# Kernel tuning notes

Hardware: AMD Instinct MI355X
Metric: run time of the kernel (lower is better)

Reference implementation:

```python
import jax, jax.numpy as jnp
import numpy as np

D_MODEL = 64  # per-head dim used for temperature


def setup_inputs() -> dict:
    key = jax.random.key(0)
    kq, kk, kv, km = jax.random.split(key, 4)
    B, S, D = 16, 2048, D_MODEL
    q = jax.random.normal(kq, (B, S, D), dtype=jnp.float32)
    k = jax.random.normal(kk, (B, S, D), dtype=jnp.float32)
    v = jax.random.normal(kv, (B, S, D), dtype=jnp.float32)
    attn_mask = jax.random.randint(km, (B, S), 0, 2).astype(bool)  # True = masked
    return {"q": q, "k": k, "v": v, "attn_mask": attn_mask}


def reference(q, k, v, attn_mask):
    temper = jnp.asarray(D_MODEL ** 0.5, dtype=q.dtype)
    # scores: [B, S_q, S_k]
    attn = jnp.einsum('bqd,bkd->bqk', q, k) / temper
    # mask broadcast over query dim (torch: unsqueeze(1).expand_as)
    attn = jnp.where(attn_mask[:, None, :], -jnp.inf, attn)
    attn = jax.nn.softmax(attn, axis=-1)
    # nan-fix: fully-masked rows produce NaN -> set to 0 (matches torch code)
    attn = jnp.where(jnp.isnan(attn), jnp.zeros((), dtype=attn.dtype), attn)
    # dropout prob is 0.0 -> identity
    output = jnp.einsum('bqk,bkd->bqd', attn, v)
    return (output, attn)
```

## Files before the change

### kernel.cpp

```cpp
#include <hip/hip_runtime.h>
#include <math.h>

constexpr int B = 16, S = 2048, D = 64;
constexpr int TK = 64;
constexpr int NT = S / TK;
constexpr float SCALE = 0.125f;
constexpr int STRH = 88;

typedef __attribute__((ext_vector_type(8))) short bf16x8;
typedef __attribute__((ext_vector_type(16))) float f32x16;

__device__ __forceinline__ unsigned short f2bf(float x) {
    union { float f; unsigned u; } c; c.f = x;
    return (unsigned short)((c.u + 0x7fff + ((c.u >> 16) & 1)) >> 16);
}
__device__ __forceinline__ float bf2f(unsigned short h) {
    union { unsigned u; float f; } c; c.u = ((unsigned)h) << 16; return c.f;
}
__device__ __forceinline__ unsigned pk2(float a, float b) {
    return (unsigned)f2bf(a) | ((unsigned)f2bf(b) << 16);
}
__device__ __forceinline__ int rowof(int h, int r) { return (r & 3) + 8 * (r >> 2) + 4 * h; }

__global__ __launch_bounds__(256)
void preconv(const float* __restrict__ q, const float* __restrict__ k,
             const float* __restrict__ v, unsigned short* __restrict__ Qb,
             unsigned short* __restrict__ Kb, unsigned short* __restrict__ Vtb)
{
    __shared__ unsigned short vt[64 * 72];
    const int b = blockIdx.x >> 5, s0 = (blockIdx.x & 31) * 64;
    const int t = threadIdx.x;

    const float4* qs = (const float4*)(q + ((size_t)b * S + s0) * D);
    const float4* ks = (const float4*)(k + ((size_t)b * S + s0) * D);
    const float4* vs = (const float4*)(v + ((size_t)b * S + s0) * D);
    unsigned* Qd = (unsigned*)(Qb + ((size_t)b * S + s0) * D);
    unsigned* Kd = (unsigned*)(Kb + ((size_t)b * S + s0) * D);

    #pragma unroll
    for (int i = 0; i < 4; ++i) {
        int f4 = t + 256 * i;
        float4 x = qs[f4];
        Qd[f4 * 2] = pk2(x.x, x.y); Qd[f4 * 2 + 1] = pk2(x.z, x.w);
        float4 y = ks[f4];
        Kd[f4 * 2] = pk2(y.x, y.y); Kd[f4 * 2 + 1] = pk2(y.z, y.w);
        float4 z = vs[f4];
        int r = f4 >> 4, cc = (f4 & 15) * 4;
        vt[(cc + 0) * 72 + r] = f2bf(z.x);
        vt[(cc + 1) * 72 + r] = f2bf(z.y);
        vt[(cc + 2) * 72 + r] = f2bf(z.z);
        vt[(cc + 3) * 72 + r] = f2bf(z.w);
    }
    __syncthreads();
    #pragma unroll
    for (int i = 0; i < 2; ++i) {
        int ch = t + 256 * i;
        int d = ch >> 3, o = ch & 7;
        int4 val = *(const int4*)&vt[d * 72 + o * 8];
        *(int4*)(Vtb + ((size_t)(b * 64 + d)) * S + s0 + o * 8) = val;
    }
}

__global__ __launch_bounds__(256)
void sdpa_v3(const unsigned short* __restrict__ Qb, const unsigned short* __restrict__ Kb,
             const unsigned short* __restrict__ Vtb, const int* __restrict__ maskg,
             float* __restrict__ outg, float* __restrict__ attng)
{
    __shared__ __align__(16) short Ks[2][TK * STRH];
    __shared__ __align__(16) short Vt[2][TK * STRH];
    __shared__ __align__(16) short Ps[64 * STRH];
    __shared__ float mfl[2][TK];
    __shared__ float rsum[2][64];

    const int t = threadIdx.x;
    const int w = t >> 6, lane = t & 63, m = lane & 31, h = lane >> 5;
    const int p = w >> 1, c = w & 1;
    const int b = blockIdx.x >> 5;
    const int q0 = (blockIdx.x & 31) * 64;

    bf16x8 aq[4];
    {
        const unsigned short* qrow = Qb + ((size_t)(b * S + q0 + 32 * p + m)) * D;
        #pragma unroll
        for (int s = 0; s < 4; ++s) aq[s] = *(const bf16x8*)(qrow + s * 16 + h * 8);
    }

    int4 kreg[2], vreg[2];
    int mreg = 0;

    auto gloadK = [&](int gk) {
        #pragma unroll
        for (int i = 0; i < 2; ++i) {
            int ch = t + 256 * i;
            kreg[i] = *(const int4*)(Kb + ((size_t)(b * S + gk + (ch >> 3))) * D + (ch & 7) * 8);
        }
        if (t < TK) mreg = maskg[b * S + gk + t];
    };
    auto gloadV = [&](int gk) {
        #pragma unroll
        for (int i = 0; i < 2; ++i) {
            int ch = t + 256 * i;
            vreg[i] = *(const int4*)(Vtb + ((size_t)(b * 64 + (ch >> 3))) * S + gk + (ch & 7) * 8);
        }
    };
    auto commitK = [&](int buf) {
        #pragma unroll
        for (int i = 0; i < 2; ++i) {
            int ch = t + 256 * i;
            *(int4*)&Ks[buf][(ch >> 3) * STRH + (ch & 7) * 8] = kreg[i];
        }
        if (t < TK) mfl[buf][t] = mreg ? 1.0f : 0.0f;
    };
    auto commitV = [&](int buf) {
        #pragma unroll
        for (int i = 0; i < 2; ++i) {
            int ch = t + 256 * i;
            *(int4*)&Vt[buf][(ch >> 3) * STRH + (ch & 7) * 8] = vreg[i];
        }
    };
    auto scores = [&](int buf, f32x16& c0) {
        #pragma unroll
        for (int i = 0; i < 16; ++i) c0[i] = 0.f;
        #pragma unroll
        for (int s = 0; s < 4; ++s) {
            bf16x8 bk = *(const bf16x8*)&Ks[buf][(32 * c + m) * STRH + s * 16 + h * 8];
            c0 = __builtin_amdgcn_mfma_f32_32x32x16_bf16(aq[s], bk, c0, 0, 0, 0);
        }
    };

    float rs[16];
    #pragma unroll
    for (int r = 0; r < 16; ++r) rs[r] = 0.f;

    gloadK(0);
    for (int t2 = 0; t2 < NT; ++t2) {
        commitK(t2 & 1);
        __syncthreads();
        if (t2 + 1 < NT) gloadK((t2 + 1) * TK);
        f32x16 c0; scores(t2 & 1, c0);
        float mk = mfl[t2 & 1][32 * c + m];
        #pragma unroll
        for (int r = 0; r < 16; ++r)
            if (mk == 0.f) rs[r] += __expf(c0[r] * SCALE);
    }
    #pragma unroll
    for (int off = 1; off < 32; off <<= 1)
        #pragma unroll
        for (int r = 0; r < 16; ++r) rs[r] += __shfl_xor(rs[r], off, 64);
    if (m == 0) {
        #pragma unroll
        for (int r = 0; r < 16; ++r) rsum[c][32 * p + rowof(h, r)] = rs[r];
    }
    __syncthreads();
    float rli[16];
    #pragma unroll
    for (int r = 0; r < 16; ++r) {
        int row = 32 * p + rowof(h, r);
        float tot = rsum[0][row] + rsum[1][row];
        rli[r] = tot > 0.f ? 1.f / tot : 0.f;
    }

    f32x16 o;
    #pragma unroll
    for (int i = 0; i < 16; ++i) o[i] = 0.f;

    gloadK(0); gloadV(0);
    for (int t2 = 0; t2 < NT; ++t2) {
        const int gk = t2 * TK;
        const int buf = t2 & 1;
        commitK(buf); commitV(buf);
        __syncthreads();
        if (t2 + 1 < NT) { gloadK(gk + TK); gloadV(gk + TK); }

        f32x16 c0; scores(buf, c0);
        float mk = mfl[buf][32 * c + m];
        #pragma unroll
        for (int r = 0; r < 16; ++r) {
            float pv = (mk == 0.f) ? __expf(c0[r] * SCALE) * rli[r] : 0.f;
            Ps[(32 * p + rowof(h, r)) * STRH + 32 * c + m] = (short)f2bf(pv);
        }
        __syncthreads();

        float* ab = attng + ((size_t)(b * S + q0)) * S + gk;
        #pragma unroll
        for (int i = 0; i < 2; ++i) {
            int ch = t + 256 * i;
            int rr = ch >> 3, o8 = ch & 7;
            bf16x8 pv8 = *(const bf16x8*)&Ps[rr * STRH + o8 * 8];
            float4 f0 = make_float4(bf2f(pv8[0]), bf2f(pv8[1]), bf2f(pv8[2]), bf2f(pv8[3]));
            float4 f1 = make_float4(bf2f(pv8[4]), bf2f(pv8[5]), bf2f(pv8[6]), bf2f(pv8[7]));
            float* dst = ab + (size_t)rr * S + o8 * 8;
            *(float4*)dst = f0; *(float4*)(dst + 4) = f1;
        }
        #pragma unroll
        for (int kk = 0; kk < 4; ++kk) {
            bf16x8 ap = *(const bf16x8*)&Ps[(32 * p + m) * STRH + kk * 16 + h * 8];
            bf16x8 bv = *(const bf16x8*)&Vt[buf][(32 * c + m) * STRH + kk * 16 + h * 8];
            o = __builtin_amdgcn_mfma_f32_32x32x16_bf16(ap, bv, o, 0, 0, 0);
        }
    }

    #pragma unroll
    for (int r = 0; r < 16; ++r)
        outg[((size_t)(b * S + q0 + 32 * p + rowof(h, r))) * D + 32 * c + m] = o[r];
}

__global__ __launch_bounds__(256)
void sdpa_fb(const float* __restrict__ qg, const float* __restrict__ kg,
             const float* __restrict__ vg, const int* __restrict__ maskg,
             float* __restrict__ outg, float* __restrict__ attng)
{
    constexpr int FSTR = 72;
    __shared__ __align__(16) short Qs[128 * FSTR];
    __shared__ __align__(16) short KsF[64 * FSTR];
    __shared__ __align__(16) short VtF[64 * FSTR];
    __shared__ __align__(16) short PsF[4 * 32 * FSTR];
    __shared__ float mflag[64];

    const int t = threadIdx.x;
    const int w = t >> 6, lane = t & 63, m = lane & 31, half = lane >> 5;
    const int b = blockIdx.x >> 4;
    const int q0 = (blockIdx.x & 15) * 128;

    {
        const float4* src = (const float4*)(qg + ((size_t)b * S + q0) * D);
        #pragma unroll
        for (int i = 0; i < 8; ++i) {
            int f4 = t + i * 256;
            float4 v = src[f4];
            unsigned* dst = (unsigned*)&Qs[(f4 >> 4) * FSTR + (f4 & 15) * 4];
            dst[0] = pk2(v.x, v.y); dst[1] = pk2(v.z, v.w);
        }
    }
    __syncthreads();
    bf16x8 aq[4];
    #pragma unroll
    for (int s = 0; s < 4; ++s)
        aq[s] = *(const bf16x8*)&Qs[(w * 32 + m) * FSTR + s * 16 + half * 8];

    auto stageK = [&](int gk) {
        const float4* src = (const float4*)(kg + ((size_t)b * S + gk) * D);
        #pragma unroll
        for (int i = 0; i < 4; ++i) {
            int f4 = t + i * 256;
            float4 v = src[f4];
            unsigned* dst = (unsigned*)&KsF[(f4 >> 4) * FSTR + (f4 & 15) * 4];
            dst[0] = pk2(v.x, v.y); dst[1] = pk2(v.z, v.w);
        }
        if (t < 64) mflag[t] = maskg[b * S + gk + t] ? 1.0f : 0.0f;
    };
    auto stageV = [&](int gk) {
        const float4* src = (const float4*)(vg + ((size_t)b * S + gk) * D);
        #pragma unroll
        for (int i = 0; i < 4; ++i) {
            int f4 = t + i * 256;
            float4 v = src[f4];
            int r = f4 >> 4, cc = (f4 & 15) * 4;
            VtF[(cc + 0) * FSTR + r] = (short)f2bf(v.x);
            VtF[(cc + 1) * FSTR + r] = (short)f2bf(v.y);
            VtF[(cc + 2) * FSTR + r] = (short)f2bf(v.z);
            VtF[(cc + 3) * FSTR + r] = (short)f2bf(v.w);
        }
    };
    auto scoresF = [&](f32x16& c0, f32x16& c1) {
        #pragma unroll
        for (int i = 0; i < 16; ++i) { c0[i] = 0.f; c1[i] = 0.f; }
        #pragma unroll
        for (int s = 0; s < 4; ++s) {
            bf16x8 b0 = *(const bf16x8*)&KsF[m * FSTR + s * 16 + half * 8];
            bf16x8 b1 = *(const bf16x8*)&KsF[(32 + m) * FSTR + s * 16 + half * 8];
            c0 = __builtin_amdgcn_mfma_f32_32x32x16_bf16(aq[s], b0, c0, 0, 0, 0);
            c1 = __builtin_amdgcn_mfma_f32_32x32x16_bf16(aq[s], b1, c1, 0, 0, 0);
        }
    };

    float rs[16];
    #pragma unroll
    for (int r = 0; r < 16; ++r) rs[r] = 0.f;
    for (int tile = 0; tile < NT; ++tile) {
        stageK(tile * TK);
        __syncthreads();
        f32x16 c0, c1; scoresF(c0, c1);
        float mk0 = mflag[m], mk1 = mflag[32 + m];
        #pragma unroll
        for (int r = 0; r < 16; ++r) {
            float p0 = (mk0 == 0.f) ? __expf(c0[r] * SCALE) : 0.f;
            float p1 = (mk1 == 0.f) ? __expf(c1[r] * SCALE) : 0.f;
            rs[r] += p0 + p1;
        }
        __syncthreads();
    }
    #pragma unroll
    for (int off = 1; off < 32; off <<= 1)
        #pragma unroll
        for (int r = 0; r < 16; ++r) rs[r] += __shfl_xor(rs[r], off, 64);
    float rli[16];
    #pragma unroll
    for (int r = 0; r < 16; ++r) rli[r] = rs[r] > 0.f ? 1.f / rs[r] : 0.f;

    f32x16 o0, o1;
    #pragma unroll
    for (int i = 0; i < 16; ++i) { o0[i] = 0.f; o1[i] = 0.f; }
    short* Pw = &PsF[w * 32 * FSTR];
    float* abase = attng + ((size_t)(b * S + q0 + w * 32)) * S;

    for (int tile = 0; tile < NT; ++tile) {
        const int gk = tile * TK;
        stageK(gk); stageV(gk);
        __syncthreads();
        f32x16 c0, c1; scoresF(c0, c1);
        float mk0 = mflag[m], mk1 = mflag[32 + m];
        #pragma unroll
        for (int r = 0; r < 16; ++r) {
            int row = rowof(half, r);
            float p0 = (mk0 == 0.f) ? __expf(c0[r] * SCALE) * rli[r] : 0.f;
            float p1 = (mk1 == 0.f) ? __expf(c1[r] * SCALE) * rli[r] : 0.f;
            Pw[row * FSTR + m]      = (short)f2bf(p0);
            Pw[row * FSTR + 32 + m] = (short)f2bf(p1);
        }
        #pragma unroll
        for (int i = 0; i < 16; ++i) {
            int row = i * 2 + half;
            unsigned u = *(const unsigned*)&Pw[row * FSTR + 2 * m];
            float2 val = make_float2(bf2f((unsigned short)(u & 0xffff)),
                                     bf2f((unsigned short)(u >> 16)));
            *(float2*)&abase[(size_t)row * S + gk + 2 * m] = val;
        }
        #pragma unroll
        for (int kk = 0; kk < 4; ++kk) {
            bf16x8 ap  = *(const bf16x8*)&Pw[m * FSTR + kk * 16 + half * 8];
            bf16x8 bv0 = *(const bf16x8*)&VtF[m * FSTR + kk * 16 + half * 8];
            bf16x8 bv1 = *(const bf16x8*)&VtF[(32 + m) * FSTR + kk * 16 + half * 8];
            o0 = __builtin_amdgcn_mfma_f32_32x32x16_bf16(ap, bv0, o0, 0, 0, 0);
            o1 = __builtin_amdgcn_mfma_f32_32x32x16_bf16(ap, bv1, o1, 0, 0, 0);
        }
        __syncthreads();
    }
    float* obase = outg + ((size_t)(b * S + q0 + w * 32)) * D;
    #pragma unroll
    for (int r = 0; r < 16; ++r) {
        int row = rowof(half, r);
        obase[row * D + m]      = o0[r];
        obase[row * D + 32 + m] = o1[r];
    }
}

extern "C" void kernel_launch(void* const* d_in, const int* in_sizes, int n_in,
                              void* d_out, int out_size, void* d_ws, size_t ws_size,
                              hipStream_t stream) {
    const float* q    = (const float*)d_in[0];
    const float* k    = (const float*)d_in[1];
    const float* v    = (const float*)d_in[2];
    const int*   mask = (const int*)d_in[3];

    float* out  = (float*)d_out;
    float* attn = (float*)d_out + (size_t)B * S * D;

    const size_t elems = (size_t)B * S * D;
    const size_t need  = 3 * elems * sizeof(unsigned short);

    if (ws_size >= need) {
        unsigned short* Qb  = (unsigned short*)d_ws;
        unsigned short* Kb  = Qb + elems;
        unsigned short* Vtb = Kb + elems;
        preconv<<<dim3(B * (S / 64)), dim3(256), 0, stream>>>(q, k, v, Qb, Kb, Vtb);
        sdpa_v3<<<dim3(B * (S / 64)), dim3(256), 0, stream>>>(Qb, Kb, Vtb, mask, out, attn);
    } else {
        sdpa_fb<<<dim3(B * (S / 128)), dim3(256), 0, stream>>>(q, k, v, mask, out, attn);
    }
}
```

Before: 376.0 us.

## Split key range across waves per 32-query tile, dropping LDS staging for K/V

Replaces the 64-query block kernel with one that handles 32 query rows per block, with each of the four waves covering a quarter of the key range. K and V are read directly from global memory with no LDS double buffering, and the waves no longer synchronise with each other inside the loop. Partial row sums and partial outputs are reduced across waves through LDS at the end, and normalisation moves to the attention store and the final output. It also remaps block IDs, uses nontemporal stores for the large attention matrix and sets launch bounds for occupancy. The trade-off is more redundant global K/V reads in exchange for fewer barriers and higher occupancy.

Result: slower. 538.2 us (+43.1%).

```diff
diff --git a/kernel.cpp b/kernel.cpp
--- a/kernel.cpp
+++ b/kernel.cpp
@@ -5,9 +5,9 @@
 constexpr int TK = 64;
 constexpr int NT = S / TK;
 constexpr float SCALE = 0.125f;
-constexpr int STRH = 88;
 
 typedef __attribute__((ext_vector_type(8))) short bf16x8;
+typedef __attribute__((ext_vector_type(4))) float f32x4;
 typedef __attribute__((ext_vector_type(16))) float f32x16;
 
 __device__ __forceinline__ unsigned short f2bf(float x) {
@@ -61,87 +61,62 @@
     }
 }
 
-__global__ __launch_bounds__(256)
-void sdpa_v3(const unsigned short* __restrict__ Qb, const unsigned short* __restrict__ Kb,
+constexpr int TQ2  = 32;
+constexpr int KW2  = S / 4;
+constexpr int TK2  = 32;
+constexpr int NT2  = KW2 / TK2;
+constexpr int PSTR = 40;
+
+__global__ __launch_bounds__(256, 4)
+void sdpa_v4(const unsigned short* __restrict__ Qb, const unsigned short* __restrict__ Kb,
              const unsigned short* __restrict__ Vtb, const int* __restrict__ maskg,
              float* __restrict__ outg, float* __restrict__ attng)
 {
-    __shared__ __align__(16) short Ks[2][TK * STRH];
-    __shared__ __align__(16) short Vt[2][TK * STRH];
-    __shared__ __align__(16) short Ps[64 * STRH];
-    __shared__ float mfl[2][TK];
-    __shared__ float rsum[2][64];
+    __shared__ __align__(16) float smem[4 * TQ2 * D];
+    __shared__ float rsum[4][TQ2];
+    __shared__ float tot[TQ2];
 
     const int t = threadIdx.x;
     const int w = t >> 6, lane = t & 63, m = lane & 31, h = lane >> 5;
-    const int p = w >> 1, c = w & 1;
-    const int b = blockIdx.x >> 5;
-    const int q0 = (blockIdx.x & 31) * 64;
+    int bid = (int)blockIdx.x;
+    bid = (bid & 7) * 128 + (bid >> 3);
+    const int b  = bid >> 6;
+    const int q0 = (bid & 63) * TQ2;
+    const int k0 = w * KW2;
+
+    const unsigned short* Kbase = Kb  + (size_t)b * S * D;
+    const unsigned short* Vbase = Vtb + (size_t)b * D * S;
+    const int* mbase = maskg + b * S;
+    short* Psw = reinterpret_cast<short*>(smem) + w * (TQ2 * PSTR);
 
     bf16x8 aq[4];
     {
-        const unsigned short* qrow = Qb + ((size_t)(b * S + q0 + 32 * p + m)) * D;
-        #pragma unroll
-        for (int s = 0; s < 4; ++s) aq[s] = *(const bf16x8*)(qrow + s * 16 + h * 8);
-    }
-
-    int4 kreg[2], vreg[2];
-    int mreg = 0;
-
-    auto gloadK = [&](int gk) {
-        #pragma unroll
-        for (int i = 0; i < 2; ++i) {
-            int ch = t + 256 * i;
-            kreg[i] = *(const int4*)(Kb + ((size_t)(b * S + gk + (ch >> 3))) * D + (ch & 7) * 8);
-        }
-        if (t < TK) mreg = maskg[b * S + gk + t];
-    };
-    auto gloadV = [&](int gk) {
-        #pragma unroll
-        for (int i = 0; i < 2; ++i) {
-            int ch = t + 256 * i;
-            vreg[i] = *(const int4*)(Vtb + ((size_t)(b * 64 + (ch >> 3))) * S + gk + (ch & 7) * 8);
-        }
-    };
-    auto commitK = [&](int buf) {
-        #pragma unroll
-        for (int i = 0; i < 2; ++i) {
-            int ch = t + 256 * i;
-            *(int4*)&Ks[buf][(ch >> 3) * STRH + (ch & 7) * 8] = kreg[i];
-        }
-        if (t < TK) mfl[buf][t] = mreg ? 1.0f : 0.0f;
-    };
-    auto commitV = [&](int buf) {
-        #pragma unroll
-        for (int i = 0; i < 2; ++i) {
-            int ch = t + 256 * i;
-            *(int4*)&Vt[buf][(ch >> 3) * STRH + (ch & 7) * 8] = vreg[i];
-        }
-    };
-    auto scores = [&](int buf, f32x16& c0) {
-        #pragma unroll
-        for (int i = 0; i < 16; ++i) c0[i] = 0.f;
+        const unsigned short* qrow = Qb + ((size_t)(b * S + q0 + m)) * D + h * 8;
+        #pragma unroll
+        for (int s = 0; s < 4; ++s) aq[s] = *(const bf16x8*)(qrow + s * 16);
+    }
+
+    float rs[16];
+    #pragma unroll
+    for (int r = 0; r < 16; ++r) rs[r] = 0.f;
+
+    #pragma unroll 2
+    for (int it = 0; it < NT2; ++it) {
+        const int gk = k0 + it * TK2;
+        const int mk = mbase[gk + m];
+        const unsigned short* krow = Kbase + (size_t)(gk + m) * D + h * 8;
+        f32x16 c;
+        #pragma unroll
+        for (int i = 0; i < 16; ++i) c[i] = 0.f;
         #pragma unroll
         for (int s = 0; s < 4; ++s) {
-            bf16x8 bk = *(const bf16x8*)&Ks[buf][(32 * c + m) * STRH + s * 16 + h * 8];
-            c0 = __builtin_amdgcn_mfma_f32_32x32x16_bf16(aq[s], bk, c0, 0, 0, 0);
-        }
-    };
-
-    float rs[16];
-    #pragma unroll
-    for (int r = 0; r < 16; ++r) rs[r] = 0.f;
-
-    gloadK(0);
-    for (int t2 = 0; t2 < NT; ++t2) {
-        commitK(t2 & 1);
-        __syncthreads();
-        if (t2 + 1 < NT) gloadK((t2 + 1) * TK);
-        f32x16 c0; scores(t2 & 1, c0);
-        float mk = mfl[t2 & 1][32 * c + m];
-        #pragma unroll
-        for (int r = 0; r < 16; ++r)
-            if (mk == 0.f) rs[r] += __expf(c0[r] * SCALE);
+            bf16x8 bk = *(const bf16x8*)(krow + s * 16);
+            c = __builtin_amdgcn_mfma_f32_32x32x16_bf16(aq[s], bk, c, 0, 0, 0);
+        }
+        if (mk == 0) {
+            #pragma unroll
+            for (int r = 0; r < 16; ++r) rs[r] += __expf(c[r] * SCALE);
+        }
     }
     #pragma unroll
     for (int off = 1; off < 32; off <<= 1)
@@ -149,60 +124,95 @@
         for (int r = 0; r < 16; ++r) rs[r] += __shfl_xor(rs[r], off, 64);
     if (m == 0) {
         #pragma unroll
-        for (int r = 0; r < 16; ++r) rsum[c][32 * p + rowof(h, r)] = rs[r];
-    }
-    __syncthreads();
-    float rli[16];
-    #pragma unroll
-    for (int r = 0; r < 16; ++r) {
-        int row = 32 * p + rowof(h, r);
-        float tot = rsum[0][row] + rsum[1][row];
-        rli[r] = tot > 0.f ? 1.f / tot : 0.f;
-    }
-
-    f32x16 o;
-    #pragma unroll
-    for (int i = 0; i < 16; ++i) o[i] = 0.f;
-
-    gloadK(0); gloadV(0);
-    for (int t2 = 0; t2 < NT; ++t2) {
-        const int gk = t2 * TK;
-        const int buf = t2 & 1;
-        commitK(buf); commitV(buf);
-        __syncthreads();
-        if (t2 + 1 < NT) { gloadK(gk + TK); gloadV(gk + TK); }
-
-        f32x16 c0; scores(buf, c0);
-        float mk = mfl[buf][32 * c + m];
+        for (int r = 0; r < 16; ++r) rsum[w][rowof(h, r)] = rs[r];
+    }
+    __syncthreads();
+    if (t < TQ2) tot[t] = rsum[0][t] + rsum[1][t] + rsum[2][t] + rsum[3][t];
+    __syncthreads();
+    const float tm = tot[m];
+    const float rli_m = tm > 0.f ? 1.f / tm : 0.f;
+
+    f32x16 o0, o1;
+    #pragma unroll
+    for (int i = 0; i < 16; ++i) { o0[i] = 0.f; o1[i] = 0.f; }
+
+    #pragma unroll 2
+    for (int it = 0; it < NT2; ++it) {
+        const int gk = k0 + it * TK2;
+        const int mk = mbase[gk + m];
+        const unsigned short* krow = Kbase + (size_t)(gk + m) * D + h * 8;
+        f32x16 c;
+        #pragma unroll
+        for (int i = 0; i < 16; ++i) c[i] = 0.f;
+        #pragma unroll
+        for (int s = 0; s < 4; ++s) {
+            bf16x8 bk = *(const bf16x8*)(krow + s * 16);
+            c = __builtin_amdgcn_mfma_f32_32x32x16_bf16(aq[s], bk, c, 0, 0, 0);
+        }
+        if (mk == 0) {
+            #pragma unroll
+            for (int r = 0; r < 16; ++r)
+                Psw[rowof(h, r) * PSTR + m] = (short)f2bf(__expf(c[r] * SCALE));
+        } else {
+            #pragma unroll
+            for (int r = 0; r < 16; ++r) Psw[rowof(h, r) * PSTR + m] = 0;
+        }
+
+        #pragma unroll
+        for (int kk = 0; kk < 2; ++kk) {
+            bf16x8 ap  = *(const bf16x8*)&Psw[m * PSTR + kk * 16 + h * 8];
+            bf16x8 bv0 = *(const bf16x8*)(Vbase + (size_t)m * S + gk + kk * 16 + h * 8);
+            bf16x8 bv1 = *(const bf16x8*)(Vbase + (size_t)(32 + m) * S + gk + kk * 16 + h * 8);
+            o0 = __builtin_amdgcn_mfma_f32_32x32x16_bf16(ap, bv0, o0, 0, 0, 0);
+            o1 = __builtin_amdgcn_mfma_f32_32x32x16_bf16(ap, bv1, o1, 0, 0, 0);
+        }
+
+        {
+            const short* pr = &Psw[m * PSTR + h * 16];
+            bf16x8 p0 = *(const bf16x8*)pr;
+            bf16x8 p1 = *(const bf16x8*)(pr + 8);
+            float* ab = attng + ((size_t)(b * S + q0 + m)) * S + gk + h * 16;
+            f32x4 f0 = { bf2f((unsigned short)p0[0]) * rli_m, bf2f((unsigned short)p0[1]) * rli_m,
+                         bf2f((unsigned short)p0[2]) * rli_m, bf2f((unsigned short)p0[3]) * rli_m };
+            f32x4 f1 = { bf2f((unsigned short)p0[4]) * rli_m, bf2f((unsigned short)p0[5]) * rli_m,
+                         bf2f((unsigned short)p0[6]) * rli_m, bf2f((unsigned short)p0[7]) * rli_m };
+            f32x4 f2 = { bf2f((unsigned short)p1[0]) * rli_m, bf2f((unsigned short)p1[1]) * rli_m,
+                         bf2f((unsigned short)p1[2]) * rli_m, bf2f((unsigned short)p1[3]) * rli_m };
+            f32x4 f3 = { bf2f((unsigned short)p1[4]) * rli_m, bf2f((unsigned short)p1[5]) * rli_m,
+                         bf2f((unsigned short)p1[6]) * rli_m, bf2f((unsigned short)p1[7]) * rli_m };
+            __builtin_nontemporal_store(f0, (f32x4*)ab);
+            __builtin_nontemporal_store(f1, (f32x4*)(ab + 4));
+            __builtin_nontemporal_store(f2, (f32x4*)(ab + 8));
+            __builtin_nontemporal_store(f3, (f32x4*)(ab + 12));
+        }
+    }
+
+    __syncthreads();
+    {
+        float* Ocw = smem + w * (TQ2 * D);
         #pragma unroll
         for (int r = 0; r < 16; ++r) {
-            float pv = (mk == 0.f) ? __expf(c0[r] * SCALE) * rli[r] : 0.f;
-            Ps[(32 * p + rowof(h, r)) * STRH + 32 * c + m] = (short)f2bf(pv);
-        }
-        __syncthreads();
-
-        float* ab = attng + ((size_t)(b * S + q0)) * S + gk;
+            const int row = rowof(h, r);
+            Ocw[row * D + m]      = o0[r];
+            Ocw[row * D + 32 + m] = o1[r];
+        }
+    }
+    __syncthreads();
+    {
+        float* ob = outg + ((size_t)(b * S + q0)) * D;
         #pragma unroll
         for (int i = 0; i < 2; ++i) {
-            int ch = t + 256 * i;
-            int rr = ch >> 3, o8 = ch & 7;
-            bf16x8 pv8 = *(const bf16x8*)&Ps[rr * STRH + o8 * 8];
-            float4 f0 = make_float4(bf2f(pv8[0]), bf2f(pv8[1]), bf2f(pv8[2]), bf2f(pv8[3]));
-            float4 f1 = make_float4(bf2f(pv8[4]), bf2f(pv8[5]), bf2f(pv8[6]), bf2f(pv8[7]));
-            float* dst = ab + (size_t)rr * S + o8 * 8;
-            *(float4*)dst = f0; *(float4*)(dst + 4) = f1;
-        }
-        #pragma unroll
-        for (int kk = 0; kk < 4; ++kk) {
-            bf16x8 ap = *(const bf16x8*)&Ps[(32 * p + m) * STRH + kk * 16 + h * 8];
-            bf16x8 bv = *(const bf16x8*)&Vt[buf][(32 * c + m) * STRH + kk * 16 + h * 8];
-            o = __builtin_amdgcn_mfma_f32_32x32x16_bf16(ap, bv, o, 0, 0, 0);
-        }
-    }
-
-    #pragma unroll
-    for (int r = 0; r < 16; ++r)
-        outg[((size_t)(b * S + q0 + 32 * p + rowof(h, r))) * D + 32 * c + m] = o[r];
+            const int i4 = t * 2 + i;
+            f32x4 a0 = *(const f32x4*)&smem[0 * TQ2 * D + i4 * 4];
+            f32x4 a1 = *(const f32x4*)&smem[1 * TQ2 * D + i4 * 4];
+            f32x4 a2 = *(const f32x4*)&smem[2 * TQ2 * D + i4 * 4];
+            f32x4 a3 = *(const f32x4*)&smem[3 * TQ2 * D + i4 * 4];
+            const float tr = tot[i4 >> 4];
+            const float sc = tr > 0.f ? 1.f / tr : 0.f;
+            f32x4 sum = (a0 + a1 + a2 + a3) * sc;
+            *(f32x4*)&ob[i4 * 4] = sum;
+        }
+    }
 }
 
 __global__ __launch_bounds__(256)
@@ -364,7 +374,7 @@
         unsigned short* Kb  = Qb + elems;
         unsigned short* Vtb = Kb + elems;
         preconv<<<dim3(B * (S / 64)), dim3(256), 0, stream>>>(q, k, v, Qb, Kb, Vtb);
-        sdpa_v3<<<dim3(B * (S / 64)), dim3(256), 0, stream>>>(Qb, Kb, Vtb, mask, out, attn);
+        sdpa_v4<<<dim3(B * (S / TQ2)), dim3(256), 0, stream>>>(Qb, Kb, Vtb, mask, out, attn);
     } else {
         sdpa_fb<<<dim3(B * (S / 128)), dim3(256), 0, stream>>>(q, k, v, mask, out, attn);
     }
```

## Double key tile to 128 and reuse V buffer as second K buffer in pass one

Applied to the files above, without the earlier changes.

The key tile grows from 64 to 128 keys, so each wave computes two 32x32 score blocks per tile and the loops run half as many iterations, with half as many barriers. Shared memory is re-partitioned: the first pass aliases a V buffer as its second K double-buffer, while the second pass single-buffers K and double-buffers V. The attention-row store now writes one float4 per thread per chunk instead of two. Register pressure rises from larger staging arrays and two accumulators, which may reduce occupancy, and single-buffered K in pass two relies on the barrier ordering.

New measurement: 401.1 us. 1.07x slower.

```diff
diff --git a/kernel.cpp b/kernel.cpp
--- a/kernel.cpp
+++ b/kernel.cpp
@@ -2,10 +2,14 @@
 #include <math.h>
 
 constexpr int B = 16, S = 2048, D = 64;
-constexpr int TK = 64;
+constexpr int TK = 128;
 constexpr int NT = S / TK;
+constexpr int TKF = 64;
+constexpr int NTF = S / TKF;
 constexpr float SCALE = 0.125f;
-constexpr int STRH = 88;
+constexpr int KSTR = 72;
+constexpr int VSTR = 136;
+constexpr int PSTR = 136;
 
 typedef __attribute__((ext_vector_type(8))) short bf16x8;
 typedef __attribute__((ext_vector_type(16))) float f32x16;
@@ -62,13 +66,13 @@
 }
 
 __global__ __launch_bounds__(256)
-void sdpa_v3(const unsigned short* __restrict__ Qb, const unsigned short* __restrict__ Kb,
+void sdpa_v7(const unsigned short* __restrict__ Qb, const unsigned short* __restrict__ Kb,
              const unsigned short* __restrict__ Vtb, const int* __restrict__ maskg,
              float* __restrict__ outg, float* __restrict__ attng)
 {
-    __shared__ __align__(16) short Ks[2][TK * STRH];
-    __shared__ __align__(16) short Vt[2][TK * STRH];
-    __shared__ __align__(16) short Ps[64 * STRH];
+    __shared__ __align__(16) short Ks[TK * KSTR];
+    __shared__ __align__(16) short Vt[2][64 * VSTR];
+    __shared__ __align__(16) short Ps[64 * PSTR];
     __shared__ float mfl[2][TK];
     __shared__ float rsum[2][64];
 
@@ -85,12 +89,12 @@
         for (int s = 0; s < 4; ++s) aq[s] = *(const bf16x8*)(qrow + s * 16 + h * 8);
     }
 
-    int4 kreg[2], vreg[2];
+    int4 kreg[4], vreg[4];
     int mreg = 0;
 
     auto gloadK = [&](int gk) {
         #pragma unroll
-        for (int i = 0; i < 2; ++i) {
+        for (int i = 0; i < 4; ++i) {
             int ch = t + 256 * i;
             kreg[i] = *(const int4*)(Kb + ((size_t)(b * S + gk + (ch >> 3))) * D + (ch & 7) * 8);
         }
@@ -98,35 +102,40 @@
     };
     auto gloadV = [&](int gk) {
         #pragma unroll
-        for (int i = 0; i < 2; ++i) {
-            int ch = t + 256 * i;
-            vreg[i] = *(const int4*)(Vtb + ((size_t)(b * 64 + (ch >> 3))) * S + gk + (ch & 7) * 8);
-        }
-    };
-    auto commitK = [&](int buf) {
-        #pragma unroll
-        for (int i = 0; i < 2; ++i) {
-            int ch = t + 256 * i;
-            *(int4*)&Ks[buf][(ch >> 3) * STRH + (ch & 7) * 8] = kreg[i];
-        }
-        if (t < TK) mfl[buf][t] = mreg ? 1.0f : 0.0f;
+        for (int i = 0; i < 4; ++i) {
+            int ch = t + 256 * i;
+            vreg[i] = *(const int4*)(Vtb + ((size_t)(b * 64 + (ch >> 4))) * S + gk + (ch & 15) * 8);
+        }
+    };
+    auto commitK = [&](short* kb, float* mf) {
+        #pragma unroll
+        for (int i = 0; i < 4; ++i) {
+            int ch = t + 256 * i;
+            *(int4*)&kb[(ch >> 3) * KSTR + (ch & 7) * 8] = kreg[i];
+        }
+        if (t < TK) mf[t] = mreg ? 1.0f : 0.0f;
     };
     auto commitV = [&](int buf) {
         #pragma unroll
-        for (int i = 0; i < 2; ++i) {
-            int ch = t + 256 * i;
-            *(int4*)&Vt[buf][(ch >> 3) * STRH + (ch & 7) * 8] = vreg[i];
-        }
-    };
-    auto scores = [&](int buf, f32x16& c0) {
-        #pragma unroll
-        for (int i = 0; i < 16; ++i) c0[i] = 0.f;
+        for (int i = 0; i < 4; ++i) {
+            int ch = t + 256 * i;
+            *(int4*)&Vt[buf][(ch >> 4) * VSTR + (ch & 15) * 8] = vreg[i];
+        }
+    };
+    auto scores = [&](const short* kb, f32x16& c0, f32x16& c1) {
+        #pragma unroll
+        for (int i = 0; i < 16; ++i) { c0[i] = 0.f; c1[i] = 0.f; }
         #pragma unroll
         for (int s = 0; s < 4; ++s) {
-            bf16x8 bk = *(const bf16x8*)&Ks[buf][(32 * c + m) * STRH + s * 16 + h * 8];
-            c0 = __builtin_amdgcn_mfma_f32_32x32x16_bf16(aq[s], bk, c0, 0, 0, 0);
-        }
-    };
+            bf16x8 b0 = *(const bf16x8*)&kb[(32 * c + m) * KSTR + s * 16 + h * 8];
+            bf16x8 b1 = *(const bf16x8*)&kb[(32 * c + 64 + m) * KSTR + s * 16 + h * 8];
+            c0 = __builtin_amdgcn_mfma_f32_32x32x16_bf16(aq[s], b0, c0, 0, 0, 0);
+            c1 = __builtin_amdgcn_mfma_f32_32x32x16_bf16(aq[s], b1, c1, 0, 0, 0);
+        }
+    };
+
+    short* kb0 = Ks;
+    short* kb1 = &Vt[0][0];
 
     float rs[16];
     #pragma unroll
@@ -134,14 +143,18 @@
 
     gloadK(0);
     for (int t2 = 0; t2 < NT; ++t2) {
-        commitK(t2 & 1);
+        short* kb = (t2 & 1) ? kb1 : kb0;
+        commitK(kb, mfl[t2 & 1]);
         __syncthreads();
         if (t2 + 1 < NT) gloadK((t2 + 1) * TK);
-        f32x16 c0; scores(t2 & 1, c0);
-        float mk = mfl[t2 & 1][32 * c + m];
-        #pragma unroll
-        for (int r = 0; r < 16; ++r)
-            if (mk == 0.f) rs[r] += __expf(c0[r] * SCALE);
+        f32x16 c0, c1; scores(kb, c0, c1);
+        float mk0 = mfl[t2 & 1][32 * c + m];
+        float mk1 = mfl[t2 & 1][32 * c + 64 + m];
+        #pragma unroll
+        for (int r = 0; r < 16; ++r) {
+            if (mk0 == 0.f) rs[r] += __expf(c0[r] * SCALE);
+            if (mk1 == 0.f) rs[r] += __expf(c1[r] * SCALE);
+        }
     }
     #pragma unroll
     for (int off = 1; off < 32; off <<= 1)
@@ -168,34 +181,37 @@
     for (int t2 = 0; t2 < NT; ++t2) {
         const int gk = t2 * TK;
         const int buf = t2 & 1;
-        commitK(buf); commitV(buf);
+        commitK(Ks, mfl[0]); commitV(buf);
         __syncthreads();
         if (t2 + 1 < NT) { gloadK(gk + TK); gloadV(gk + TK); }
 
-        f32x16 c0; scores(buf, c0);
-        float mk = mfl[buf][32 * c + m];
+        f32x16 c0, c1; scores(Ks, c0, c1);
+        float mk0 = mfl[0][32 * c + m];
+        float mk1 = mfl[0][32 * c + 64 + m];
         #pragma unroll
         for (int r = 0; r < 16; ++r) {
-            float pv = (mk == 0.f) ? __expf(c0[r] * SCALE) * rli[r] : 0.f;
-            Ps[(32 * p + rowof(h, r)) * STRH + 32 * c + m] = (short)f2bf(pv);
+            float p0 = (mk0 == 0.f) ? __expf(c0[r] * SCALE) * rli[r] : 0.f;
+            float p1 = (mk1 == 0.f) ? __expf(c1[r] * SCALE) * rli[r] : 0.f;
+            int row = 32 * p + rowof(h, r);
+            Ps[row * PSTR + 32 * c + m]      = (short)f2bf(p0);
+            Ps[row * PSTR + 32 * c + 64 + m] = (short)f2bf(p1);
         }
         __syncthreads();
 
         float* ab = attng + ((size_t)(b * S + q0)) * S + gk;
         #pragma unroll
-        for (int i = 0; i < 2; ++i) {
-            int ch = t + 256 * i;
-            int rr = ch >> 3, o8 = ch & 7;
-            bf16x8 pv8 = *(const bf16x8*)&Ps[rr * STRH + o8 * 8];
-            float4 f0 = make_float4(bf2f(pv8[0]), bf2f(pv8[1]), bf2f(pv8[2]), bf2f(pv8[3]));
-            float4 f1 = make_float4(bf2f(pv8[4]), bf2f(pv8[5]), bf2f(pv8[6]), bf2f(pv8[7]));
-            float* dst = ab + (size_t)rr * S + o8 * 8;
-            *(float4*)dst = f0; *(float4*)(dst + 4) = f1;
-        }
-        #pragma unroll
-        for (int kk = 0; kk < 4; ++kk) {
-            bf16x8 ap = *(const bf16x8*)&Ps[(32 * p + m) * STRH + kk * 16 + h * 8];
-            bf16x8 bv = *(const bf16x8*)&Vt[buf][(32 * c + m) * STRH + kk * 16 + h * 8];
+        for (int i = 0; i < 8; ++i) {
+            int ch = t + 256 * i;
+            int rr = ch >> 5, cq = ch & 31;
+            short4 pv4 = *(const short4*)&Ps[rr * PSTR + cq * 4];
+            float4 f = make_float4(bf2f((unsigned short)pv4.x), bf2f((unsigned short)pv4.y),
+                                   bf2f((unsigned short)pv4.z), bf2f((unsigned short)pv4.w));
+            *(float4*)(ab + (size_t)rr * S + cq * 4) = f;
+        }
+        #pragma unroll
+        for (int kk = 0; kk < 8; ++kk) {
+            bf16x8 ap = *(const bf16x8*)&Ps[(32 * p + m) * PSTR + kk * 16 + h * 8];
+            bf16x8 bv = *(const bf16x8*)&Vt[buf][(32 * c + m) * VSTR + kk * 16 + h * 8];
             o = __builtin_amdgcn_mfma_f32_32x32x16_bf16(ap, bv, o, 0, 0, 0);
         }
     }
@@ -277,8 +293,8 @@
     float rs[16];
     #pragma unroll
     for (int r = 0; r < 16; ++r) rs[r] = 0.f;
-    for (int tile = 0; tile < NT; ++tile) {
-        stageK(tile * TK);
+    for (int tile = 0; tile < NTF; ++tile) {
+        stageK(tile * TKF);
         __syncthreads();
         f32x16 c0, c1; scoresF(c0, c1);
         float mk0 = mflag[m], mk1 = mflag[32 + m];
@@ -304,8 +320,8 @@
     short* Pw = &PsF[w * 32 * FSTR];
     float* abase = attng + ((size_t)(b * S + q0 + w * 32)) * S;
 
-    for (int tile = 0; tile < NT; ++tile) {
-        const int gk = tile * TK;
+    for (int tile = 0; tile < NTF; ++tile) {
+        const int gk = tile * TKF;
         stageK(gk); stageV(gk);
         __syncthreads();
         f32x16 c0, c1; scoresF(c0, c1);
@@ -364,7 +380,7 @@
         unsigned short* Kb  = Qb + elems;
         unsigned short* Vtb = Kb + elems;
         preconv<<<dim3(B * (S / 64)), dim3(256), 0, stream>>>(q, k, v, Qb, Kb, Vtb);
-        sdpa_v3<<<dim3(B * (S / 64)), dim3(256), 0, stream>>>(Qb, Kb, Vtb, mask, out, attn);
+        sdpa_v7<<<dim3(B * (S / 64)), dim3(256), 0, stream>>>(Qb, Kb, Vtb, mask, out, attn);
     } else {
         sdpa_fb<<<dim3(B * (S / 128)), dim3(256), 0, stream>>>(q, k, v, mask, out, attn);
     }
```
